# Optimization experiments

Hardware: AMD Instinct MI355X
Metric: run time of the kernel (lower is better)

## Reference

```python
import jax, jax.numpy as jnp
import numpy as np

B, T, D, H = 2, 2048, 512, 8
HD = D // H
EPS = 1e-5


def setup_inputs() -> dict:
    key = jax.random.key(0)
    ks = jax.random.split(key, 8)
    s = 1.0 / np.sqrt(D)
    return {
        "x": jax.random.normal(ks[0], (B, T, D), dtype=jnp.float32),
        "Wq": jax.random.uniform(ks[1], (D, D), jnp.float32, -s, s),
        "bq": jnp.zeros((D,), jnp.float32),
        "Wk": jax.random.uniform(ks[2], (D, D), jnp.float32, -s, s),
        "bk": jnp.zeros((D,), jnp.float32),
        "Wv": jax.random.uniform(ks[3], (D, D), jnp.float32, -s, s),
        "bv": jnp.zeros((D,), jnp.float32),
        "gn_w": jnp.ones((D,), jnp.float32),
        "gn_b": jnp.zeros((D,), jnp.float32),
        "gamma": jnp.float32(0.9),
    }


def reference(x, Wq, bq, Wk, bk, Wv, bv, gn_w, gn_b, gamma):
    Bx, Tx, Dx = x.shape
    # projections (torch Linear: x @ W.T + b), split heads -> [B,H,T,hd]
    def proj(W, b):
        return (x @ W.T + b).reshape(Bx, Tx, H, HD).transpose(0, 2, 1, 3)
    Q, K, V = proj(Wq, bq), proj(Wk, bk), proj(Wv, bv)
    # retention scores with causal exponential decay mask
    attn = jnp.einsum("bhqd,bhkd->bhqk", Q, K)  # [B,H,T,T]
    idx = jnp.arange(Tx)
    diff = idx[:, None] - idx[None, :]
    # clamp negative exponents before pow to avoid inf (masked out anyway)
    decay = jnp.where(diff >= 0,
                      jnp.power(gamma, jnp.maximum(diff, 0).astype(jnp.float32)),
                      0.0)
    attn = attn * decay[None, None]
    out = jnp.einsum("bhqk,bhkd->bhqd", attn, V)  # [B,H,T,hd]
    out = out.transpose(0, 2, 1, 3)  # [B,T,H,hd]
    # GroupNorm over channels grouped by head; normalized over (T, hd) per (b, h)
    mean = out.mean(axis=(1, 3), keepdims=True)
    var = out.var(axis=(1, 3), keepdims=True)
    out = (out - mean) / jnp.sqrt(var + EPS)
    out = out.reshape(Bx, Tx, Dx) * gn_w + gn_b
    return out
```

## Files before the change

kernel.cpp:

```cpp
#include <hip/hip_runtime.h>
#include <math.h>

#define B_ 2
#define T_ 2048
#define D_ 512
#define H_ 8
#define HD_ 64
#define NG_ (B_*H_)
#define EPS_ 1e-5f

typedef __attribute__((ext_vector_type(8)))  short  short8;
typedef __attribute__((ext_vector_type(16))) float  floatx16;

__device__ inline floatx16 zero16() {
    floatx16 z;
#pragma unroll
    for (int i = 0; i < 16; i++) z[i] = 0.f;
    return z;
}

__device__ inline unsigned pack2bf(float a, float b) {
    unsigned ua = __float_as_uint(a), ub = __float_as_uint(b);
    ua = (ua + 0x7fffu + ((ua >> 16) & 1u)) >> 16;
    ub = (ub + 0x7fffu + ((ub >> 16) & 1u)) >> 16;
    return ua | (ub << 16);
}
__device__ inline short bf1(float a) {
    unsigned ua = __float_as_uint(a);
    return (short)((ua + 0x7fffu + ((ua >> 16) & 1u)) >> 16);
}

__global__ __launch_bounds__(256) void convert_kernel(
    const float* __restrict__ x,
    const float* __restrict__ Wq, const float* __restrict__ Wk, const float* __restrict__ Wv,
    short* __restrict__ xb, short* __restrict__ Wb)
{
    const int XN = 4096 * 512;
    const int WN = 512 * 512;
    size_t e = ((size_t)blockIdx.x * 256 + threadIdx.x) * 8;
    const float* src; short* dst;
    if (e < XN)               { src = x  + e;               dst = xb + e; }
    else if (e < XN + WN)     { src = Wq + (e - XN);        dst = Wb + (e - XN); }
    else if (e < XN + 2*WN)   { src = Wk + (e - XN - WN);   dst = Wb + (e - XN); }
    else                      { src = Wv + (e - XN - 2*WN); dst = Wb + (e - XN); }
    float4 a = *(const float4*)src;
    float4 b = *(const float4*)(src + 4);
    uint4 o;
    o.x = pack2bf(a.x, a.y); o.y = pack2bf(a.z, a.w);
    o.z = pack2bf(b.x, b.y); o.w = pack2bf(b.z, b.w);
    *(uint4*)dst = o;
}

__global__ __launch_bounds__(256) void proj_mfma(
    const short* __restrict__ xb, const short* __restrict__ Wb,
    const float* __restrict__ bq, const float* __restrict__ bk, const float* __restrict__ bv,
    short* __restrict__ Qo, short* __restrict__ Ko, short* __restrict__ Vto)
{
    __shared__ short Xs[128 * 64];
    __shared__ short Ws2[128 * 64];

    const int tid = threadIdx.x;
    const int w = tid >> 6, lane = tid & 63;
    const int hi = lane >> 5, ln = lane & 31;
    const int mt0 = blockIdx.x * 128;
    const int nt0 = blockIdx.y * 128;
    const int z = blockIdx.z;
    const bool isV = (z == 2);
    const float* bias = (z == 0) ? bq : (z == 1) ? bk : bv;
    const short* Wz = Wb + (size_t)z * 512 * 512;

    const int srow = w * 32 + (lane >> 3);
    const int scol = (lane & 7) * 8;
    const int mh = w & 1, nh = w >> 1;

    floatx16 acc[2][2] = {{zero16(), zero16()}, {zero16(), zero16()}};

    for (int k0 = 0; k0 < 512; k0 += 64) {
        __syncthreads();
#pragma unroll
        for (int c = 0; c < 4; c++) {
            const short* gx = xb + (size_t)(mt0 + srow + c * 8) * 512 + k0 + scol;
            const short* gw = Wz + (size_t)(nt0 + srow + c * 8) * 512 + k0 + scol;
            short* lx = Xs  + (w * 32 + c * 8) * 64;
            short* lw = Ws2 + (w * 32 + c * 8) * 64;
            __builtin_amdgcn_global_load_lds(
                (const __attribute__((address_space(1))) unsigned*)gx,
                (__attribute__((address_space(3))) unsigned*)lx, 16, 0, 0);
            __builtin_amdgcn_global_load_lds(
                (const __attribute__((address_space(1))) unsigned*)gw,
                (__attribute__((address_space(3))) unsigned*)lw, 16, 0, 0);
        }
        __syncthreads();

#pragma unroll
        for (int kk = 0; kk < 4; kk++) {
            short8 xf[2], wf[2];
#pragma unroll
            for (int s = 0; s < 2; s++) {
                xf[s] = *(const short8*)(Xs  + (mh * 64 + s * 32 + ln) * 64 + kk * 16 + hi * 8);
                wf[s] = *(const short8*)(Ws2 + (nh * 64 + s * 32 + ln) * 64 + kk * 16 + hi * 8);
            }
#pragma unroll
            for (int a = 0; a < 2; a++)
#pragma unroll
                for (int b = 0; b < 2; b++)
                    acc[a][b] = isV
                        ? __builtin_amdgcn_mfma_f32_32x32x16_bf16(wf[a], xf[b], acc[a][b], 0, 0, 0)
                        : __builtin_amdgcn_mfma_f32_32x32x16_bf16(xf[a], wf[b], acc[a][b], 0, 0, 0);
        }
    }

    const int head = blockIdx.y * 2 + nh;

    if (!isV) {
        short* dst = (z == 0) ? Qo : Ko;
        float bias_v[2];
#pragma unroll
        for (int b = 0; b < 2; b++) bias_v[b] = bias[nt0 + nh * 64 + b * 32 + ln];
#pragma unroll
        for (int a = 0; a < 2; a++) {
            const int mbase = mt0 + mh * 64 + a * 32;
#pragma unroll
            for (int r = 0; r < 16; r++) {
                int m = mbase + (r & 3) + 8 * (r >> 2) + 4 * hi;
                int batch = m >> 11, t = m & (T_ - 1);
                size_t rowb = ((size_t)(batch * H_ + head) * T_ + t) * HD_;
#pragma unroll
                for (int b = 0; b < 2; b++)
                    dst[rowb + b * 32 + ln] = bf1(acc[a][b][r] + bias_v[b]);
            }
        }
    } else {
#pragma unroll
        for (int a = 0; a < 2; a++) {
#pragma unroll
            for (int r = 0; r < 16; r++) {
                int chan = nt0 + nh * 64 + a * 32 + (r & 3) + 8 * (r >> 2) + 4 * hi;
                int d = chan & (HD_ - 1);
                float bv_ = bias[chan];
#pragma unroll
                for (int b = 0; b < 2; b++) {
                    int m = mt0 + mh * 64 + b * 32 + ln;
                    int batch = m >> 11, t = m & (T_ - 1);
                    Vto[((size_t)(batch * H_ + head) * HD_ + d) * T_ + t] = bf1(acc[a][b][r] + bv_);
                }
            }
        }
    }
}

__global__ __launch_bounds__(256) void retention_kernel(
    const short* __restrict__ Q, const short* __restrict__ K, const short* __restrict__ Vt,
    const float* __restrict__ gamma_p,
    float* __restrict__ out,
    float* __restrict__ stats)
{
    __shared__ float red[2][32 * 64];

    const int tid  = threadIdx.x;
    const int w    = tid >> 6, lane = tid & 63;
    const int qh   = w & 1,  ks  = w >> 1;
    const int hi   = lane >> 5, ln = lane & 31;
    const int qt   = blockIdx.x, g = blockIdx.y;
    const int q0   = qt * 64;

    const float gamma = gamma_p[0];
    const float lg = logf(gamma);
    int kt0 = 0;
    if (lg < -1e-6f) {
        int maxd = (int)(-34.0f / lg) + 64;
        kt0 = qt - (maxd >> 6);
        if (kt0 < 0) kt0 = 0;
    }

    const short* Qbase = Q + ((size_t)g * T_ + q0 + qh * 32 + ln) * HD_;
    short8 qf[4];
#pragma unroll
    for (int c = 0; c < 4; c++) qf[c] = *(const short8*)(Qbase + 16 * c + 8 * hi);

    const float Alane = __expf(lg * (float)(qh * 32 + ln - 4 * hi));
    const float G32   = __expf(-lg * 32.0f);
    float Er[16];
#pragma unroll
    for (int r = 0; r < 16; r++) Er[r] = __expf(-lg * (float)((r & 3) + 8 * (r >> 2)));

    floatx16 oacc[2] = {zero16(), zero16()};

    for (int kt = kt0 + ((ks - kt0) & 1); kt <= qt; kt += 2) {
        const int k0 = kt * 64;
        const short* Kbase = K + ((size_t)g * T_ + k0) * HD_;

        floatx16 st[2];
#pragma unroll
        for (int kh = 0; kh < 2; kh++) {
            const short* kp = Kbase + (size_t)(kh * 32 + ln) * HD_ + 8 * hi;
            floatx16 acc = zero16();
#pragma unroll
            for (int c = 0; c < 4; c++) {
                short8 a = *(const short8*)(kp + 16 * c);
                acc = __builtin_amdgcn_mfma_f32_32x32x16_bf16(a, qf[c], acc, 0, 0, 0);
            }
            st[kh] = acc;
        }

        const float Ckt = __expf(lg * (float)(q0 - k0));
        const float base0 = Alane * Ckt;
        const bool diag = (kt == qt);
#pragma unroll
        for (int kh = 0; kh < 2; kh++) {
            float bb = base0 * (kh ? G32 : 1.0f);
#pragma unroll
            for (int r = 0; r < 16; r++) {
                float v = st[kh][r] * (bb * Er[r]);
                if (diag) {
                    int kloc = kh * 32 + (r & 3) + 8 * (r >> 2) + 4 * hi;
                    int qloc = qh * 32 + ln;
                    if (qloc < kloc) v = 0.f;
                }
                st[kh][r] = v;
            }
        }

#pragma unroll
        for (int c = 0; c < 4; c++) {
            const int kh = c >> 1, rb = 8 * (c & 1);
            unsigned p0 = pack2bf(st[kh][rb+0], st[kh][rb+1]);
            unsigned p1 = pack2bf(st[kh][rb+2], st[kh][rb+3]);
            unsigned p2 = pack2bf(st[kh][rb+4], st[kh][rb+5]);
            unsigned p3 = pack2bf(st[kh][rb+6], st[kh][rb+7]);
            unsigned t0s = (unsigned)__shfl_xor((int)(hi ? p0 : p2), 32, 64);
            unsigned t1s = (unsigned)__shfl_xor((int)(hi ? p1 : p3), 32, 64);
            uint4 aw;
            aw.x = hi ? t0s : p0;  aw.y = hi ? t1s : p1;
            aw.z = hi ? p2  : t0s; aw.w = hi ? p3  : t1s;
            short8 afr = *reinterpret_cast<short8*>(&aw);
#pragma unroll
            for (int dh = 0; dh < 2; dh++) {
                const short* vp = Vt + ((size_t)g * HD_ + dh * 32 + ln) * T_ + k0 + 16 * c + 8 * hi;
                short8 bfr = *(const short8*)vp;
                oacc[dh] = __builtin_amdgcn_mfma_f32_32x32x16_bf16(afr, bfr, oacc[dh], 0, 0, 0);
            }
        }
    }

    float* rp = &red[qh][0];
    if (ks == 1) {
#pragma unroll
        for (int dh = 0; dh < 2; dh++)
#pragma unroll
            for (int r = 0; r < 16; r++) {
                int qloc = (r & 3) + 8 * (r >> 2) + 4 * hi;
                rp[qloc * 64 + dh * 32 + ln] = oacc[dh][r];
            }
    }
    __syncthreads();
    if (ks == 0) {
        const int b = g >> 3, h = g & 7;
        float sm = 0.f, sq = 0.f;
#pragma unroll
        for (int dh = 0; dh < 2; dh++)
#pragma unroll
            for (int r = 0; r < 16; r++) {
                int qloc = (r & 3) + 8 * (r >> 2) + 4 * hi;
                float v = oacc[dh][r] + rp[qloc * 64 + dh * 32 + ln];
                int q = q0 + qh * 32 + qloc;
                out[((size_t)(b * T_ + q)) * D_ + h * 64 + dh * 32 + ln] = v;
                sm += v; sq += v * v;
            }
        for (int off = 32; off > 0; off >>= 1) {
            sm += __shfl_down(sm, off);
            sq += __shfl_down(sq, off);
        }
        if (lane == 0) {
            atomicAdd(&stats[g], sm);
            atomicAdd(&stats[NG_ + g], sq);
        }
    }
}

__global__ __launch_bounds__(256) void norm_kernel(
    float* __restrict__ out, const float* __restrict__ stats,
    const float* __restrict__ gn_w, const float* __restrict__ gn_b)
{
    int idx = blockIdx.x * 256 + threadIdx.x;
    if (idx >= B_ * T_ * D_) return;
    int c = idx & (D_ - 1);
    int b = idx >> 20;
    int g = b * H_ + (c >> 6);
    const float invN = 1.f / (float)(T_ * HD_);
    float mean = stats[g] * invN;
    float var  = stats[NG_ + g] * invN - mean * mean;
    float inv  = rsqrtf(var + EPS_);
    out[idx] = (out[idx] - mean) * inv * gn_w[c] + gn_b[c];
}

extern "C" void kernel_launch(void* const* d_in, const int* in_sizes, int n_in,
                              void* d_out, int out_size, void* d_ws, size_t ws_size,
                              hipStream_t stream)
{
    const float* x    = (const float*)d_in[0];
    const float* Wq   = (const float*)d_in[1];
    const float* bq   = (const float*)d_in[2];
    const float* Wk   = (const float*)d_in[3];
    const float* bk   = (const float*)d_in[4];
    const float* Wv   = (const float*)d_in[5];
    const float* bv   = (const float*)d_in[6];
    const float* gn_w = (const float*)d_in[7];
    const float* gn_b = (const float*)d_in[8];
    const float* gam  = (const float*)d_in[9];
    float* out = (float*)d_out;

    const size_t per = (size_t)B_ * H_ * T_ * HD_;
    float* stats = (float*)d_ws;
    short* Qw  = (short*)((char*)d_ws + 256);
    short* Kw  = Qw + per;
    short* Vtw = Kw + per;
    short* xb  = Vtw + per;
    short* Wb  = xb + per;

    hipMemsetAsync(stats, 0, 256, stream);
    convert_kernel<<<1408, 256, 0, stream>>>(x, Wq, Wk, Wv, xb, Wb);
    proj_mfma<<<dim3(32, 4, 3), 256, 0, stream>>>(xb, Wb, bq, bk, bv, Qw, Kw, Vtw);
    retention_kernel<<<dim3(32, 16), 256, 0, stream>>>(Qw, Kw, Vtw, gam, out, stats);
    norm_kernel<<<8192, 256, 0, stream>>>(out, stats, gn_w, gn_b);
}
```

Baseline: 140.7 us.

## Halve tile heights and split retention key range across four waves

The projection kernel now uses 64-row M tiles, doubling the grid so more CUs have work. The retention kernel now gives each block 32 query rows, with all four waves striding over key tiles by four and reducing partials through shared memory. V fragments are prefetched before the decay/mask step, and a min-blocks hint is added. This adds parallelism for the small problem in exchange for redundant K/V reads, a larger reduction, and extra per-tile loop overhead.

Measured after the change: 139.2 us. No clear change (-1.0%).

```diff
diff --git a/kernel.cpp b/kernel.cpp
--- a/kernel.cpp
+++ b/kernel.cpp
@@ -56,36 +56,39 @@
     const float* __restrict__ bq, const float* __restrict__ bk, const float* __restrict__ bv,
     short* __restrict__ Qo, short* __restrict__ Ko, short* __restrict__ Vto)
 {
-    __shared__ short Xs[128 * 64];
+    __shared__ short Xs[64 * 64];
     __shared__ short Ws2[128 * 64];
 
     const int tid = threadIdx.x;
     const int w = tid >> 6, lane = tid & 63;
     const int hi = lane >> 5, ln = lane & 31;
-    const int mt0 = blockIdx.x * 128;
+    const int mt0 = blockIdx.x * 64;
     const int nt0 = blockIdx.y * 128;
     const int z = blockIdx.z;
     const bool isV = (z == 2);
     const float* bias = (z == 0) ? bq : (z == 1) ? bk : bv;
     const short* Wz = Wb + (size_t)z * 512 * 512;
 
-    const int srow = w * 32 + (lane >> 3);
-    const int scol = (lane & 7) * 8;
+    const int srow = tid >> 3;
+    const int scol = (tid & 7) * 8;
     const int mh = w & 1, nh = w >> 1;
 
-    floatx16 acc[2][2] = {{zero16(), zero16()}, {zero16(), zero16()}};
+    floatx16 acc[2] = {zero16(), zero16()};
 
     for (int k0 = 0; k0 < 512; k0 += 64) {
         __syncthreads();
 #pragma unroll
-        for (int c = 0; c < 4; c++) {
-            const short* gx = xb + (size_t)(mt0 + srow + c * 8) * 512 + k0 + scol;
-            const short* gw = Wz + (size_t)(nt0 + srow + c * 8) * 512 + k0 + scol;
-            short* lx = Xs  + (w * 32 + c * 8) * 64;
-            short* lw = Ws2 + (w * 32 + c * 8) * 64;
+        for (int i = 0; i < 2; i++) {
+            const short* gx = xb + (size_t)(mt0 + srow + i * 32) * 512 + k0 + scol;
+            short* lx = Xs + (srow + i * 32) * 64 + scol;
             __builtin_amdgcn_global_load_lds(
                 (const __attribute__((address_space(1))) unsigned*)gx,
                 (__attribute__((address_space(3))) unsigned*)lx, 16, 0, 0);
+        }
+#pragma unroll
+        for (int i = 0; i < 4; i++) {
+            const short* gw = Wz + (size_t)(nt0 + srow + i * 32) * 512 + k0 + scol;
+            short* lw = Ws2 + (srow + i * 32) * 64 + scol;
             __builtin_amdgcn_global_load_lds(
                 (const __attribute__((address_space(1))) unsigned*)gw,
                 (__attribute__((address_space(3))) unsigned*)lw, 16, 0, 0);
@@ -94,19 +97,16 @@
 
 #pragma unroll
         for (int kk = 0; kk < 4; kk++) {
-            short8 xf[2], wf[2];
-#pragma unroll
-            for (int s = 0; s < 2; s++) {
-                xf[s] = *(const short8*)(Xs  + (mh * 64 + s * 32 + ln) * 64 + kk * 16 + hi * 8);
+            short8 xf = *(const short8*)(Xs + (mh * 32 + ln) * 64 + kk * 16 + hi * 8);
+            short8 wf[2];
+#pragma unroll
+            for (int s = 0; s < 2; s++)
                 wf[s] = *(const short8*)(Ws2 + (nh * 64 + s * 32 + ln) * 64 + kk * 16 + hi * 8);
-            }
-#pragma unroll
-            for (int a = 0; a < 2; a++)
-#pragma unroll
-                for (int b = 0; b < 2; b++)
-                    acc[a][b] = isV
-                        ? __builtin_amdgcn_mfma_f32_32x32x16_bf16(wf[a], xf[b], acc[a][b], 0, 0, 0)
-                        : __builtin_amdgcn_mfma_f32_32x32x16_bf16(xf[a], wf[b], acc[a][b], 0, 0, 0);
+#pragma unroll
+            for (int b = 0; b < 2; b++)
+                acc[b] = isV
+                    ? __builtin_amdgcn_mfma_f32_32x32x16_bf16(wf[b], xf, acc[b], 0, 0, 0)
+                    : __builtin_amdgcn_mfma_f32_32x32x16_bf16(xf, wf[b], acc[b], 0, 0, 0);
         }
     }
 
@@ -118,51 +118,43 @@
 #pragma unroll
         for (int b = 0; b < 2; b++) bias_v[b] = bias[nt0 + nh * 64 + b * 32 + ln];
 #pragma unroll
-        for (int a = 0; a < 2; a++) {
-            const int mbase = mt0 + mh * 64 + a * 32;
+        for (int r = 0; r < 16; r++) {
+            int m = mt0 + mh * 32 + (r & 3) + 8 * (r >> 2) + 4 * hi;
+            int batch = m >> 11, t = m & (T_ - 1);
+            size_t rowb = ((size_t)(batch * H_ + head) * T_ + t) * HD_;
+#pragma unroll
+            for (int b = 0; b < 2; b++)
+                dst[rowb + b * 32 + ln] = bf1(acc[b][r] + bias_v[b]);
+        }
+    } else {
+        const int m = mt0 + mh * 32 + ln;
+        const int batch = m >> 11, t = m & (T_ - 1);
+#pragma unroll
+        for (int b = 0; b < 2; b++) {
 #pragma unroll
             for (int r = 0; r < 16; r++) {
-                int m = mbase + (r & 3) + 8 * (r >> 2) + 4 * hi;
-                int batch = m >> 11, t = m & (T_ - 1);
-                size_t rowb = ((size_t)(batch * H_ + head) * T_ + t) * HD_;
-#pragma unroll
-                for (int b = 0; b < 2; b++)
-                    dst[rowb + b * 32 + ln] = bf1(acc[a][b][r] + bias_v[b]);
-            }
-        }
-    } else {
-#pragma unroll
-        for (int a = 0; a < 2; a++) {
-#pragma unroll
-            for (int r = 0; r < 16; r++) {
-                int chan = nt0 + nh * 64 + a * 32 + (r & 3) + 8 * (r >> 2) + 4 * hi;
+                int chan = nt0 + nh * 64 + b * 32 + (r & 3) + 8 * (r >> 2) + 4 * hi;
                 int d = chan & (HD_ - 1);
-                float bv_ = bias[chan];
-#pragma unroll
-                for (int b = 0; b < 2; b++) {
-                    int m = mt0 + mh * 64 + b * 32 + ln;
-                    int batch = m >> 11, t = m & (T_ - 1);
-                    Vto[((size_t)(batch * H_ + head) * HD_ + d) * T_ + t] = bf1(acc[a][b][r] + bv_);
-                }
-            }
-        }
-    }
-}
-
-__global__ __launch_bounds__(256) void retention_kernel(
+                Vto[((size_t)(batch * H_ + head) * HD_ + d) * T_ + t] = bf1(acc[b][r] + bias[chan]);
+            }
+        }
+    }
+}
+
+__global__ __launch_bounds__(256, 3) void retention_kernel(
     const short* __restrict__ Q, const short* __restrict__ K, const short* __restrict__ Vt,
     const float* __restrict__ gamma_p,
     float* __restrict__ out,
     float* __restrict__ stats)
 {
-    __shared__ float red[2][32 * 64];
+    __shared__ float red[3][32 * 64];
 
     const int tid  = threadIdx.x;
-    const int w    = tid >> 6, lane = tid & 63;
-    const int qh   = w & 1,  ks  = w >> 1;
+    const int ks   = tid >> 6, lane = tid & 63;
     const int hi   = lane >> 5, ln = lane & 31;
-    const int qt   = blockIdx.x, g = blockIdx.y;
-    const int q0   = qt * 64;
+    const int qtt  = blockIdx.x, g = blockIdx.y;
+    const int q0   = qtt * 32;
+    const int qt   = qtt >> 1;
 
     const float gamma = gamma_p[0];
     const float lg = logf(gamma);
@@ -173,20 +165,21 @@
         if (kt0 < 0) kt0 = 0;
     }
 
-    const short* Qbase = Q + ((size_t)g * T_ + q0 + qh * 32 + ln) * HD_;
+    const short* Qbase = Q + ((size_t)g * T_ + q0 + ln) * HD_;
     short8 qf[4];
 #pragma unroll
     for (int c = 0; c < 4; c++) qf[c] = *(const short8*)(Qbase + 16 * c + 8 * hi);
 
-    const float Alane = __expf(lg * (float)(qh * 32 + ln - 4 * hi));
+    const float Alane = __expf(lg * (float)(ln - 4 * hi));
     const float G32   = __expf(-lg * 32.0f);
-    float Er[16];
-#pragma unroll
-    for (int r = 0; r < 16; r++) Er[r] = __expf(-lg * (float)((r & 3) + 8 * (r >> 2)));
+    float Ea[4], Eb[4];
+#pragma unroll
+    for (int j = 0; j < 4; j++) { Ea[j] = __expf(-lg * (float)j); Eb[j] = __expf(-lg * (float)(8 * j)); }
+    const int qrel = (qtt & 1) * 32 + ln;
 
     floatx16 oacc[2] = {zero16(), zero16()};
 
-    for (int kt = kt0 + ((ks - kt0) & 1); kt <= qt; kt += 2) {
+    for (int kt = kt0 + ((ks - kt0) & 3); kt <= qt; kt += 4) {
         const int k0 = kt * 64;
         const short* Kbase = K + ((size_t)g * T_ + k0) * HD_;
 
@@ -203,6 +196,13 @@
             st[kh] = acc;
         }
 
+        short8 vf[4][2];
+#pragma unroll
+        for (int c = 0; c < 4; c++)
+#pragma unroll
+            for (int dh = 0; dh < 2; dh++)
+                vf[c][dh] = *(const short8*)(Vt + ((size_t)g * HD_ + dh * 32 + ln) * T_ + k0 + 16 * c + 8 * hi);
+
         const float Ckt = __expf(lg * (float)(q0 - k0));
         const float base0 = Alane * Ckt;
         const bool diag = (kt == qt);
@@ -211,11 +211,10 @@
             float bb = base0 * (kh ? G32 : 1.0f);
 #pragma unroll
             for (int r = 0; r < 16; r++) {
-                float v = st[kh][r] * (bb * Er[r]);
+                float v = st[kh][r] * (bb * Ea[r & 3] * Eb[r >> 2]);
                 if (diag) {
                     int kloc = kh * 32 + (r & 3) + 8 * (r >> 2) + 4 * hi;
-                    int qloc = qh * 32 + ln;
-                    if (qloc < kloc) v = 0.f;
+                    if (qrel < kloc) v = 0.f;
                 }
                 st[kh][r] = v;
             }
@@ -235,16 +234,13 @@
             aw.z = hi ? p2  : t0s; aw.w = hi ? p3  : t1s;
             short8 afr = *reinterpret_cast<short8*>(&aw);
 #pragma unroll
-            for (int dh = 0; dh < 2; dh++) {
-                const short* vp = Vt + ((size_t)g * HD_ + dh * 32 + ln) * T_ + k0 + 16 * c + 8 * hi;
-                short8 bfr = *(const short8*)vp;
-                oacc[dh] = __builtin_amdgcn_mfma_f32_32x32x16_bf16(afr, bfr, oacc[dh], 0, 0, 0);
-            }
-        }
-    }
-
-    float* rp = &red[qh][0];
-    if (ks == 1) {
+            for (int dh = 0; dh < 2; dh++)
+                oacc[dh] = __builtin_amdgcn_mfma_f32_32x32x16_bf16(afr, vf[c][dh], oacc[dh], 0, 0, 0);
+        }
+    }
+
+    if (ks) {
+        float* rp = &red[ks - 1][0];
 #pragma unroll
         for (int dh = 0; dh < 2; dh++)
 #pragma unroll
@@ -262,8 +258,9 @@
 #pragma unroll
             for (int r = 0; r < 16; r++) {
                 int qloc = (r & 3) + 8 * (r >> 2) + 4 * hi;
-                float v = oacc[dh][r] + rp[qloc * 64 + dh * 32 + ln];
-                int q = q0 + qh * 32 + qloc;
+                int col = qloc * 64 + dh * 32 + ln;
+                float v = oacc[dh][r] + red[0][col] + red[1][col] + red[2][col];
+                int q = q0 + qloc;
                 out[((size_t)(b * T_ + q)) * D_ + h * 64 + dh * 32 + ln] = v;
                 sm += v; sq += v * v;
             }
@@ -320,7 +317,7 @@
 
     hipMemsetAsync(stats, 0, 256, stream);
     convert_kernel<<<1408, 256, 0, stream>>>(x, Wq, Wk, Wv, xb, Wb);
-    proj_mfma<<<dim3(32, 4, 3), 256, 0, stream>>>(xb, Wb, bq, bk, bv, Qw, Kw, Vtw);
-    retention_kernel<<<dim3(32, 16), 256, 0, stream>>>(Qw, Kw, Vtw, gam, out, stats);
+    proj_mfma<<<dim3(64, 4, 3), 256, 0, stream>>>(xb, Wb, bq, bk, bv, Qw, Kw, Vtw);
+    retention_kernel<<<dim3(64, 16), 256, 0, stream>>>(Qw, Kw, Vtw, gam, out, stats);
     norm_kernel<<<8192, 256, 0, stream>>>(out, stats, gn_w, gn_b);
 }
```
